# Optimization experiments

Hardware: AMD Instinct MI355X
Metric: run time of the kernel (lower is better)

Reference implementation:

```python
import jax, jax.numpy as jnp
import numpy as np

B, S, N, C = 8, 256, 256, 64
NH = 8
H, W = 256, 256
D = N * C // NH  # per-head channel dim = 2048
EPS = 1e-12


def window_reverse(windows, ws, Hh, Ww, Cc):
    # windows: (B, S, N, C) -> (B, H*W, C)
    b = windows.shape[0]
    x = windows.reshape(b, Hh // ws[0], Ww // ws[1], ws[0], ws[1], Cc)
    x = x.transpose(0, 1, 3, 2, 4, 5).reshape(b, Hh, Ww, Cc).reshape(b, Hh * Ww, Cc)
    return x


def window_partition(x, ws):
    # x: (B, H, W, C) -> (B, nWin, winElems, C)
    b, hh, ww, cc = x.shape
    x = x.reshape(b, hh // ws[0], ws[0], ww // ws[1], ws[1], cc)
    return x.transpose(0, 1, 3, 2, 4, 5).reshape(b, (hh // ws[0]) * (ww // ws[1]), ws[0] * ws[1], cc)


def setup_inputs() -> dict:
    key = jax.random.key(0)
    ks = jax.random.split(key, 6)
    x = jax.random.normal(ks[0], (B, S, N, C), dtype=jnp.float32)
    qkv_w = jax.random.normal(ks[1], (4 * C, C), dtype=jnp.float32) * 0.02
    qkv_b = jnp.zeros((4 * C,), dtype=jnp.float32)
    proj_w = jax.random.normal(ks[2], (C, C), dtype=jnp.float32) * 0.02
    proj_b = jnp.zeros((C,), dtype=jnp.float32)
    temperature1 = jnp.ones((NH, 1, 1), dtype=jnp.float32)
    temperature2 = jnp.ones((NH, 1, 1), dtype=jnp.float32)
    return {"x": x, "qkv_w": qkv_w, "qkv_b": qkv_b, "proj_w": proj_w,
            "proj_b": proj_b, "temperature1": temperature1, "temperature2": temperature2}


def reference(x, qkv_w, qkv_b, proj_w, proj_b, temperature1, temperature2):
    b, s, n, c = x.shape
    xf = x.reshape(b, s * n, c)
    # fused 4-way qkv projection (q, k, v_H, v_V)
    qkvv = (xf @ qkv_w.T + qkv_b).reshape(b, s, 4, NH, D).transpose(2, 0, 3, 1, 4)
    q, k, v_H, v_V = qkvv[0], qkvv[1], qkvv[2], qkvv[3]  # each (B, NH, S, D)

    # reorient v_V from H-windows (columns) to V-windows (rows)
    v_V = v_V.transpose(0, 2, 1, 3).reshape(b, s, n, c)       # (B,S,N,C)
    v_V = v_V.transpose(0, 2, 1, 3)                           # (B,N,S,C)
    v_V = window_reverse(v_V, (H, 1), H, W, c).reshape(b, H, W, c)
    v_V = window_partition(v_V, (1, W))                       # (B,H,W,C)
    v_V = v_V.transpose(0, 2, 1, 3)                           # (B,W,H,C) == (B,S,N,C)
    v_V = v_V.reshape(b, s, NH, D).transpose(0, 2, 1, 3)      # (B,NH,S,D)

    # cosine attention over S with per-head temperature
    qn = q / jnp.maximum(jnp.linalg.norm(q, axis=-1, keepdims=True), EPS)
    kn = k / jnp.maximum(jnp.linalg.norm(k, axis=-1, keepdims=True), EPS)
    sim = jnp.einsum('bhsd,bhtd->bhst', qn, kn)  # (B,NH,S,S)
    attn_H = jax.nn.softmax(sim * temperature1, axis=-1)
    attn_V = jax.nn.softmax(sim * temperature2, axis=-1)

    x_H = jnp.einsum('bhst,bhtd->bhsd', attn_H, v_H).transpose(0, 2, 1, 3).reshape(b, s * n, c)
    x_V = jnp.einsum('bhst,bhtd->bhsd', attn_V, v_V).transpose(0, 2, 1, 3).reshape(b, s * n, c)

    out = (x_H + x_V) @ proj_w.T + proj_b
    return out.reshape(b, s, n, c)
```

## Files before the change

### kernel.cpp

```cpp
#include <hip/hip_runtime.h>


using half_t = _Float16;
using half8 = __attribute__((ext_vector_type(8))) _Float16;
using f32x4 = __attribute__((ext_vector_type(4))) float;

#define NTOK 524288

#define GLDS(g, l) __builtin_amdgcn_global_load_lds( \
    (const __attribute__((address_space(1))) void*)(g), \
    (__attribute__((address_space(3))) void*)(l), 16, 0, 0)

#define WS_Q      0
#define WS_K      67108864
#define WS_VH     134217728
#define WS_VV     201326592
#define WS_XHV    268435456
#define WS_NQ     335544320
#define WS_NK     335609856
#define WS_WH     335675392
#define WS_WP     335708160

__global__ void kW0(const float* __restrict__ qkv_w, const float* __restrict__ proj_w,
                    half_t* __restrict__ Wh, half_t* __restrict__ Wp) {
    int tid = threadIdx.x;
    for (int i = tid; i < 256 * 64; i += 256) Wh[i] = (half_t)qkv_w[i];
    for (int i = tid; i < 64 * 64; i += 256) Wp[i] = (half_t)proj_w[i];
}

__device__ inline void y_tile_mfma(const float* __restrict__ xb,
                                   const half_t* __restrict__ Wh,
                                   int tbase, int hi, int lo,
                                   f32x4 (&acc)[4][4], int wave, int lane) {
    const int l15 = lane & 15, quad = lane >> 4;
#pragma unroll
    for (int kc = 0; kc < 2; ++kc) {
        const int c = kc * 32 + quad * 8;
        half8 afr[4];
#pragma unroll
        for (int mt = 0; mt < 4; ++mt) {
            int m = mt * 16 + l15;
            int token = tbase + (m >> 3) * hi + (m & 7) * lo;
            const float* p = xb + (size_t)token * 64 + c;
            f32x4 f0 = *(const f32x4*)p;
            f32x4 f1 = *(const f32x4*)(p + 4);
            half8 a;
            a[0] = (half_t)f0[0]; a[1] = (half_t)f0[1]; a[2] = (half_t)f0[2]; a[3] = (half_t)f0[3];
            a[4] = (half_t)f1[0]; a[5] = (half_t)f1[1]; a[6] = (half_t)f1[2]; a[7] = (half_t)f1[3];
            afr[mt] = a;
        }
#pragma unroll
        for (int i = 0; i < 4; ++i) {
            int j = (wave * 4 + i) * 16 + l15;
            half8 bfr = *(const half8*)(Wh + j * 64 + c);
#pragma unroll
            for (int mt = 0; mt < 4; ++mt)
                acc[mt][i] = __builtin_amdgcn_mfma_f32_16x16x32_f16(afr[mt], bfr, acc[mt][i], 0, 0, 0);
        }
    }
}

__device__ inline void y_dump_rowmajor(f32x4 (&acc)[4][4], const float* __restrict__ qkv_b,
                                       half_t* ylds, int wave, int lane) {
    const int l15 = lane & 15, quad = lane >> 4;
#pragma unroll
    for (int i = 0; i < 4; ++i) {
        int j = (wave * 4 + i) * 16 + l15;
        float bj = qkv_b[j];
#pragma unroll
        for (int mt = 0; mt < 4; ++mt)
#pragma unroll
            for (int r = 0; r < 4; ++r)
                ylds[(mt * 16 + quad * 4 + r) * 264 + j] = (half_t)(acc[mt][i][r] + bj);
    }
}

__device__ inline void y_dump_transposed(f32x4 (&acc)[4][4], const float* __restrict__ qkv_b,
                                         half_t* yldsT, int wave, int lane) {
    const int l15 = lane & 15, quad = lane >> 4;
#pragma unroll
    for (int i = 0; i < 4; ++i) {
        int j = (wave * 4 + i) * 16 + l15;
        float bj = qkv_b[j];
#pragma unroll
        for (int mt = 0; mt < 4; ++mt)
#pragma unroll
            for (int r = 0; r < 4; ++r)
                yldsT[j * 72 + mt * 16 + quad * 4 + r] = (half_t)(acc[mt][i][r] + bj);
    }
}

__global__ __launch_bounds__(256) void kA1(const float* __restrict__ x,
                                           const half_t* __restrict__ Wh,
                                           const float* __restrict__ qkv_b,
                                           half_t* __restrict__ Q, half_t* __restrict__ K,
                                           float* __restrict__ normQ, float* __restrict__ normK) {
    __shared__ half_t ylds[64 * 264];
    __shared__ float scr[256];
    int idx = blockIdx.x;
    int sb = idx & 31; idx >>= 5;
    int h = idx & 7; idx >>= 3;
    int g = idx & 1; int b = idx >> 1;
    int s0 = sb * 8;
    int n0 = g * 64 + h * 8;
    int tid = threadIdx.x, wave = tid >> 6, lane = tid & 63;
    const float* xb = x + (size_t)b * 65536 * 64;
    f32x4 acc[4][4];
#pragma unroll
    for (int a = 0; a < 4; ++a)
#pragma unroll
        for (int c = 0; c < 4; ++c) acc[a][c] = {0.f, 0.f, 0.f, 0.f};
    y_tile_mfma(xb, Wh, s0 * 256 + n0, 256, 1, acc, wave, lane);
    y_dump_rowmajor(acc, qkv_b, ylds, wave, lane);
    __syncthreads();
    half_t* dst = (g == 0 ? Q : K) + ((size_t)(b * 8 + h) * 256 + s0) * 2048;
    int ns = tid >> 5, jc = (tid & 31) * 8;
#pragma unroll
    for (int si = 0; si < 8; ++si) {
        half8 v = *(const half8*)&ylds[(si * 8 + ns) * 264 + jc];
        *(half8*)(dst + (size_t)si * 2048 + ns * 256 + jc) = v;
    }
    float sum = 0.f;
#pragma unroll
    for (int nn = 0; nn < 8; ++nn) {
        half8 v = *(const half8*)&ylds[((tid >> 5) * 8 + nn) * 264 + (tid & 31) * 8];
#pragma unroll
        for (int e = 0; e < 8; ++e) { float f = (float)v[e]; sum += f * f; }
    }
    scr[tid] = sum;
    __syncthreads();
    if (tid < 8) {
        float s = 0.f;
        for (int k2 = 0; k2 < 32; ++k2) s += scr[tid * 32 + k2];
        float* nd = (g == 0 ? normQ : normK);
        nd[(b * 8 + h) * 256 + s0 + tid] = s;
    }
}

__global__ __launch_bounds__(256) void kA2H(const float* __restrict__ x,
                                            const half_t* __restrict__ Wh,
                                            const float* __restrict__ qkv_b,
                                            half_t* __restrict__ VH) {
    __shared__ half_t yldsT[256 * 72];
    int idx = blockIdx.x;
    int sb = idx & 3; idx >>= 2;
    int nn = idx & 63; int b = idx >> 6;
    int h = nn >> 3, ns = nn & 7;
    int n = 128 + nn;
    int s0 = sb * 64;
    int tid = threadIdx.x, wave = tid >> 6, lane = tid & 63;
    const float* xb = x + (size_t)b * 65536 * 64;
    f32x4 acc[4][4];
#pragma unroll
    for (int a = 0; a < 4; ++a)
#pragma unroll
        for (int c = 0; c < 4; ++c) acc[a][c] = {0.f, 0.f, 0.f, 0.f};
    y_tile_mfma(xb, Wh, s0 * 256 + n, 2048, 256, acc, wave, lane);
    y_dump_transposed(acc, qkv_b, yldsT, wave, lane);
    __syncthreads();
    int jl = lane >> 3, tc = lane & 7;
    half_t* base = VH + ((size_t)(b * 8 + h) * 2048 + ns * 256) * 256 + s0 + tc * 8;
#pragma unroll
    for (int u = 0; u < 8; ++u) {
        int j = wave * 64 + u * 8 + jl;
        half8 v = *(const half8*)&yldsT[j * 72 + tc * 8];
        *(half8*)(base + (size_t)j * 256) = v;
    }
}

__global__ __launch_bounds__(256) void kA2V(const float* __restrict__ x,
                                            const half_t* __restrict__ Wh,
                                            const float* __restrict__ qkv_b,
                                            half_t* __restrict__ VV) {
    __shared__ half_t yldsT[256 * 72];
    int idx = blockIdx.x;
    int st = idx & 255; int b = idx >> 8;
    int h = st >> 5;
    int tid = threadIdx.x, wave = tid >> 6, lane = tid & 63;
    const float* xb = x + (size_t)b * 65536 * 64;
    f32x4 acc[4][4];
#pragma unroll
    for (int a = 0; a < 4; ++a)
#pragma unroll
        for (int c = 0; c < 4; ++c) acc[a][c] = {0.f, 0.f, 0.f, 0.f};
    y_tile_mfma(xb, Wh, st * 256 + 192, 8, 1, acc, wave, lane);
    y_dump_transposed(acc, qkv_b, yldsT, wave, lane);
    __syncthreads();
    int dl = lane >> 3, tc = lane & 7;
    int mbase = wave * 16 + (tc >> 2) * 8 + (tc & 3) * 2;
    half_t* base = VV + ((size_t)(b * 8 + h) * 2048 + (st & 31) * 64) * 256 + wave * 64 + tc * 8;
#pragma unroll
    for (int u = 0; u < 8; ++u) {
        int dm = u * 8 + dl;
        half8 v;
#pragma unroll
        for (int e = 0; e < 8; ++e)
            v[e] = yldsT[((e & 3) * 64 + dm) * 72 + mbase + (e >> 2)];
        *(half8*)(base + (size_t)dm * 256) = v;
    }
}

__global__ __launch_bounds__(1024, 4) void kB(const half_t* __restrict__ Q, const half_t* __restrict__ K,
                                              const half_t* __restrict__ VH, const half_t* __restrict__ VV,
                                              const float* __restrict__ normQ, const float* __restrict__ normK,
                                              const float* __restrict__ temp1, const float* __restrict__ temp2,
                                              half_t* __restrict__ xhv) {
    extern __shared__ char smem[];
    char* Ks0 = smem;
    char* Ks1 = smem + 32768;
    char* Qs0 = smem + 65536;
    char* Qs1 = smem + 73728;
    half_t* PH = (half_t*)(smem + 81920);
    half_t* PV = (half_t*)(smem + 115712);
    float* redA = (float*)(smem + 149504);
    float* redB = (float*)(smem + 153600);
    float* mH  = (float*)(smem + 157696);
    float* mV  = (float*)(smem + 157952);
    float* rHs = (float*)(smem + 158208);
    float* rVs = (float*)(smem + 158464);
    float* rq  = (float*)(smem + 158720);
    float* rk  = (float*)(smem + 158976);

    int idx = blockIdx.x;
    int bh = idx & 63;
    int sqb = idx >> 6;
    int h = bh & 7, b = bh >> 3;
    int sq0 = sqb * 64;
    int tid = threadIdx.x, wave = tid >> 6, lane = tid & 63;
    int l15 = lane & 15, quad = lane >> 4;
    float t1 = temp1[h], t2 = temp2[h];
    const half_t* Qb = Q + (size_t)bh * 256 * 2048;
    const half_t* Kb = K + (size_t)bh * 256 * 2048;
    const half_t* VHb = VH + (size_t)bh * 2048 * 256;
    const half_t* VVb = VV + (size_t)bh * 2048 * 256;

    if (tid < 64) rq[tid] = 1.f / fmaxf(sqrtf(normQ[bh * 256 + sq0 + tid]), 1e-12f);
    if (tid < 256) rk[tid] = 1.f / fmaxf(sqrtf(normK[bh * 256 + tid]), 1e-12f);

    {
        const int l7 = lane & 7, l8 = lane >> 3;
        const int swzh = (l7 ^ (l8 & 7)) * 8;
        const half_t* gK0 = Kb + (size_t)(wave * 8 + l8) * 2048 + swzh;
        const half_t* gK1 = Kb + (size_t)(128 + wave * 8 + l8) * 2048 + swzh;
        const half_t* gQ  = Qb + (size_t)(sq0 + (wave & 7) * 8 + l8) * 2048 + swzh;

        auto STAGE = [&](int kk, char* KsB, char* QsB) {
            const int off = kk * 64;
            GLDS(gK0 + off, KsB + wave * 1024);
            GLDS(gK1 + off, KsB + 16384 + wave * 1024);
            if (wave < 8) GLDS(gQ + off, QsB + wave * 1024);
        };

        f32x4 acc1[4];
#pragma unroll
        for (int a = 0; a < 4; ++a) acc1[a] = {0.f, 0.f, 0.f, 0.f};
        const int tcol = wave * 16 + l15;
        const int ts7 = tcol & 7;

        auto COMPUTE = [&](const char* KsB_, const char* QsB_) {
            const half_t* KsB = (const half_t*)KsB_;
            const half_t* QsB = (const half_t*)QsB_;
#pragma unroll
            for (int sub = 0; sub < 2; ++sub) {
                int c16 = sub * 4 + quad;
                half8 bfr = *(const half8*)(KsB + tcol * 64 + (c16 ^ ts7) * 8);
#pragma unroll
                for (int mt = 0; mt < 4; ++mt) {
                    int m = mt * 16 + l15;
                    half8 afr = *(const half8*)(QsB + m * 64 + (c16 ^ (m & 7)) * 8);
                    acc1[mt] = __builtin_amdgcn_mfma_f32_16x16x32_f16(afr, bfr, acc1[mt], 0, 0, 0);
                }
            }
        };

        STAGE(0, Ks0, Qs0);
        __syncthreads();
        for (int kk = 0; kk < 32; kk += 2) {
            if (kk + 1 < 32) STAGE(kk + 1, Ks1, Qs1);
            COMPUTE(Ks0, Qs0);
            __syncthreads();
            if (kk + 2 < 32) STAGE(kk + 2, Ks0, Qs0);
            COMPUTE(Ks1, Qs1);
            __syncthreads();
        }
        float rkt = rk[tcol];
#pragma unroll
        for (int mt = 0; mt < 4; ++mt)
#pragma unroll
            for (int r = 0; r < 4; ++r) {
                int row = mt * 16 + quad * 4 + r;
                PH[row * 264 + tcol] = (half_t)(acc1[mt][r] * rq[row] * rkt);
            }
    }
    __syncthreads();

    int r_ = tid & 63, cc = tid >> 6;
    half_t* phrow = &PH[r_ * 264 + cc * 16];
    half_t* pvrow = &PV[r_ * 264 + cc * 16];
    float mx = -3.4e38f, mn = 3.4e38f;
#pragma unroll
    for (int i2 = 0; i2 < 16; ++i2) { float v = (float)phrow[i2]; mx = fmaxf(mx, v); mn = fminf(mn, v); }
    redA[tid] = mx; redB[tid] = mn;
    __syncthreads();
    if (tid < 64) {
        float amx = -3.4e38f, amn = 3.4e38f;
#pragma unroll
        for (int q2 = 0; q2 < 16; ++q2) {
            amx = fmaxf(amx, redA[q2 * 64 + tid]);
            amn = fminf(amn, redB[q2 * 64 + tid]);
        }
        mH[tid] = (t1 >= 0.f) ? t1 * amx : t1 * amn;
        mV[tid] = (t2 >= 0.f) ? t2 * amx : t2 * amn;
    }
    __syncthreads();
    float mh = mH[r_], mv = mV[r_];
    float sh = 0.f, sv = 0.f;
#pragma unroll
    for (int i2 = 0; i2 < 16; ++i2) {
        float v = (float)phrow[i2];
        sh += __expf(v * t1 - mh);
        sv += __expf(v * t2 - mv);
    }
    redA[tid] = sh; redB[tid] = sv;
    __syncthreads();
    if (tid < 64) {
        float ash = 0.f, asv = 0.f;
#pragma unroll
        for (int q2 = 0; q2 < 16; ++q2) { ash += redA[q2 * 64 + tid]; asv += redB[q2 * 64 + tid]; }
        rHs[tid] = 1.f / ash;
        rVs[tid] = 1.f / asv;
    }
    __syncthreads();
    float rh = rHs[r_], rv = rVs[r_];
#pragma unroll
    for (int i2 = 0; i2 < 16; ++i2) {
        float v = (float)phrow[i2];
        phrow[i2] = (half_t)(__expf(v * t1 - mh) * rh);
        pvrow[i2] = (half_t)(__expf(v * t2 - mv) * rv);
    }
    __syncthreads();

#pragma unroll
    for (int i2 = 0; i2 < 2; ++i2) {
        int d0 = wave * 64 + i2 * 1024;
        f32x4 acc2[4][4];
#pragma unroll
        for (int a = 0; a < 4; ++a)
#pragma unroll
            for (int c = 0; c < 4; ++c) acc2[a][c] = {0.f, 0.f, 0.f, 0.f};
        for (int kc = 0; kc < 8; ++kc) {
            int tk = kc * 32 + quad * 8;
            half8 afr[4];
#pragma unroll
            for (int mt = 0; mt < 4; ++mt)
                afr[mt] = *(const half8*)&PH[(mt * 16 + l15) * 264 + tk];
#pragma unroll
            for (int nt = 0; nt < 4; ++nt) {
                half8 bfr = *(const half8*)(VHb + (size_t)(d0 + nt * 16 + l15) * 256 + tk);
#pragma unroll
                for (int mt = 0; mt < 4; ++mt)
                    acc2[mt][nt] = __builtin_amdgcn_mfma_f32_16x16x32_f16(afr[mt], bfr, acc2[mt][nt], 0, 0, 0);
            }
#pragma unroll
            for (int mt = 0; mt < 4; ++mt)
                afr[mt] = *(const half8*)&PV[(mt * 16 + l15) * 264 + tk];
#pragma unroll
            for (int nt = 0; nt < 4; ++nt) {
                half8 bfr = *(const half8*)(VVb + (size_t)(d0 + nt * 16 + l15) * 256 + tk);
#pragma unroll
                for (int mt = 0; mt < 4; ++mt)
                    acc2[mt][nt] = __builtin_amdgcn_mfma_f32_16x16x32_f16(afr[mt], bfr, acc2[mt][nt], 0, 0, 0);
            }
        }
        int db = wave + i2 * 16;
#pragma unroll
        for (int mt = 0; mt < 4; ++mt)
#pragma unroll
            for (int nt = 0; nt < 4; ++nt) {
                int c = nt * 16 + l15;
#pragma unroll
                for (int r = 0; r < 4; ++r) {
                    int srow = mt * 16 + quad * 4 + r;
                    size_t tk_idx = (size_t)b * 65536 + (size_t)(sq0 + srow) * 256 + h * 32 + db;
                    xhv[tk_idx * 64 + c] = (half_t)acc2[mt][nt][r];
                }
            }
    }
}

__global__ __launch_bounds__(256) void kC(const half_t* __restrict__ xhv, const half_t* __restrict__ Wp,
                                          const float* __restrict__ proj_b, float* __restrict__ out) {
    __shared__ float ot[64 * 68];
    int tid = threadIdx.x, wave = tid >> 6, lane = tid & 63;
    int l15 = lane & 15, quad = lane >> 4;
    size_t T0 = (size_t)blockIdx.x * 64;
    f32x4 acc[4];
#pragma unroll
    for (int a = 0; a < 4; ++a) acc[a] = {0.f, 0.f, 0.f, 0.f};
#pragma unroll
    for (int kc = 0; kc < 2; ++kc) {
        int c = kc * 32 + quad * 8;
        half8 bfr = *(const half8*)(Wp + (wave * 16 + l15) * 64 + c);
#pragma unroll
        for (int mt = 0; mt < 4; ++mt) {
            half8 afr = *(const half8*)(xhv + (T0 + mt * 16 + l15) * 64 + c);
            acc[mt] = __builtin_amdgcn_mfma_f32_16x16x32_f16(afr, bfr, acc[mt], 0, 0, 0);
        }
    }
    float bj = proj_b[wave * 16 + l15];
#pragma unroll
    for (int mt = 0; mt < 4; ++mt)
#pragma unroll
        for (int r = 0; r < 4; ++r)
            ot[(mt * 16 + quad * 4 + r) * 68 + wave * 16 + l15] = acc[mt][r] + bj;
    __syncthreads();
    int row = tid >> 2;
#pragma unroll
    for (int u = 0; u < 4; ++u) {
        int col = (tid & 3) * 4 + u * 16;
        f32x4 v = *(const f32x4*)&ot[row * 68 + col];
        *(f32x4*)(out + (T0 + row) * 64 + col) = v;
    }
}

extern "C" void kernel_launch(void* const* d_in, const int* in_sizes, int n_in,
                              void* d_out, int out_size, void* d_ws, size_t ws_size,
                              hipStream_t stream) {
    const float* x      = (const float*)d_in[0];
    const float* qkv_w  = (const float*)d_in[1];
    const float* qkv_b  = (const float*)d_in[2];
    const float* proj_w = (const float*)d_in[3];
    const float* proj_b = (const float*)d_in[4];
    const float* temp1  = (const float*)d_in[5];
    const float* temp2  = (const float*)d_in[6];
    char* ws = (char*)d_ws;
    half_t* Q   = (half_t*)(ws + WS_Q);
    half_t* K   = (half_t*)(ws + WS_K);
    half_t* VH  = (half_t*)(ws + WS_VH);
    half_t* VV  = (half_t*)(ws + WS_VV);
    half_t* xhv = (half_t*)(ws + WS_XHV);
    float* normQ = (float*)(ws + WS_NQ);
    float* normK = (float*)(ws + WS_NK);
    half_t* Wh  = (half_t*)(ws + WS_WH);
    half_t* Wp  = (half_t*)(ws + WS_WP);
    float* out = (float*)d_out;

    hipFuncSetAttribute((const void*)kB, hipFuncAttributeMaxDynamicSharedMemorySize, 160000);

    kW0<<<1, 256, 0, stream>>>(qkv_w, proj_w, Wh, Wp);
    kA1<<<4096, 256, 0, stream>>>(x, Wh, qkv_b, Q, K, normQ, normK);
    kA2H<<<2048, 256, 0, stream>>>(x, Wh, qkv_b, VH);
    kA2V<<<2048, 256, 0, stream>>>(x, Wh, qkv_b, VV);
    kB<<<256, 1024, 160000, stream>>>(Q, K, VH, VV, normQ, normK, temp1, temp2, xhv);
    kC<<<8192, 256, 0, stream>>>(xhv, Wp, proj_b, out);
}
```

Before: 605.9 us.

## Fuse output projection into attention kernel and use shuffle-based softmax

Removes the separate projection kernel by applying proj_w per 16-row tile inside the attention kernel, staging the fp16 tile in reused LDS and writing fp32 output directly. This eliminates the intermediate xhv buffer's global write and read and one launch. The softmax reductions now use 16-lane shuffles instead of LDS reductions with multiple barriers. The output stores become narrower per lane, and the attention kernel uses more registers.

```diff
diff --git a/kernel.cpp b/kernel.cpp
--- a/kernel.cpp
+++ b/kernel.cpp
@@ -15,7 +15,6 @@
 #define WS_K      67108864
 #define WS_VH     134217728
 #define WS_VV     201326592
-#define WS_XHV    268435456
 #define WS_NQ     335544320
 #define WS_NK     335609856
 #define WS_WH     335675392
@@ -204,22 +203,18 @@
                                               const half_t* __restrict__ VH, const half_t* __restrict__ VV,
                                               const float* __restrict__ normQ, const float* __restrict__ normK,
                                               const float* __restrict__ temp1, const float* __restrict__ temp2,
-                                              half_t* __restrict__ xhv) {
+                                              const half_t* __restrict__ Wp, const float* __restrict__ proj_b,
+                                              float* __restrict__ out) {
     extern __shared__ char smem[];
     char* Ks0 = smem;
     char* Ks1 = smem + 32768;
     char* Qs0 = smem + 65536;
     char* Qs1 = smem + 73728;
+    half_t* scratch = (half_t*)smem;
     half_t* PH = (half_t*)(smem + 81920);
     half_t* PV = (half_t*)(smem + 115712);
-    float* redA = (float*)(smem + 149504);
-    float* redB = (float*)(smem + 153600);
-    float* mH  = (float*)(smem + 157696);
-    float* mV  = (float*)(smem + 157952);
-    float* rHs = (float*)(smem + 158208);
-    float* rVs = (float*)(smem + 158464);
-    float* rq  = (float*)(smem + 158720);
-    float* rk  = (float*)(smem + 158976);
+    float* rq  = (float*)(smem + 149504);
+    float* rk  = (float*)(smem + 149760);
 
     int idx = blockIdx.x;
     int bh = idx & 63;
@@ -294,51 +289,54 @@
     }
     __syncthreads();
 
-    int r_ = tid & 63, cc = tid >> 6;
-    half_t* phrow = &PH[r_ * 264 + cc * 16];
-    half_t* pvrow = &PV[r_ * 264 + cc * 16];
-    float mx = -3.4e38f, mn = 3.4e38f;
-#pragma unroll
-    for (int i2 = 0; i2 < 16; ++i2) { float v = (float)phrow[i2]; mx = fmaxf(mx, v); mn = fminf(mn, v); }
-    redA[tid] = mx; redB[tid] = mn;
-    __syncthreads();
-    if (tid < 64) {
-        float amx = -3.4e38f, amn = 3.4e38f;
-#pragma unroll
-        for (int q2 = 0; q2 < 16; ++q2) {
-            amx = fmaxf(amx, redA[q2 * 64 + tid]);
-            amn = fminf(amn, redB[q2 * 64 + tid]);
-        }
-        mH[tid] = (t1 >= 0.f) ? t1 * amx : t1 * amn;
-        mV[tid] = (t2 >= 0.f) ? t2 * amx : t2 * amn;
-    }
-    __syncthreads();
-    float mh = mH[r_], mv = mV[r_];
-    float sh = 0.f, sv = 0.f;
-#pragma unroll
-    for (int i2 = 0; i2 < 16; ++i2) {
-        float v = (float)phrow[i2];
-        sh += __expf(v * t1 - mh);
-        sv += __expf(v * t2 - mv);
-    }
-    redA[tid] = sh; redB[tid] = sv;
-    __syncthreads();
-    if (tid < 64) {
-        float ash = 0.f, asv = 0.f;
-#pragma unroll
-        for (int q2 = 0; q2 < 16; ++q2) { ash += redA[q2 * 64 + tid]; asv += redB[q2 * 64 + tid]; }
-        rHs[tid] = 1.f / ash;
-        rVs[tid] = 1.f / asv;
-    }
-    __syncthreads();
-    float rh = rHs[r_], rv = rVs[r_];
-#pragma unroll
-    for (int i2 = 0; i2 < 16; ++i2) {
-        float v = (float)phrow[i2];
-        phrow[i2] = (half_t)(__expf(v * t1 - mh) * rh);
-        pvrow[i2] = (half_t)(__expf(v * t2 - mv) * rv);
-    }
-    __syncthreads();
+    {
+        int r_ = tid >> 4, cc = tid & 15;
+        half_t* phrow = &PH[r_ * 264 + cc * 16];
+        half_t* pvrow = &PV[r_ * 264 + cc * 16];
+        half8 v0 = *(const half8*)phrow;
+        half8 v1 = *(const half8*)(phrow + 8);
+        float fv[16];
+#pragma unroll
+        for (int e = 0; e < 8; ++e) { fv[e] = (float)v0[e]; fv[8 + e] = (float)v1[e]; }
+        float mx = fv[0], mn = fv[0];
+#pragma unroll
+        for (int e = 1; e < 16; ++e) { mx = fmaxf(mx, fv[e]); mn = fminf(mn, fv[e]); }
+#pragma unroll
+        for (int m = 1; m < 16; m <<= 1) {
+            mx = fmaxf(mx, __shfl_xor(mx, m, 16));
+            mn = fminf(mn, __shfl_xor(mn, m, 16));
+        }
+        float mh = (t1 >= 0.f) ? t1 * mx : t1 * mn;
+        float mv = (t2 >= 0.f) ? t2 * mx : t2 * mn;
+        float sh = 0.f, sv = 0.f;
+#pragma unroll
+        for (int e = 0; e < 16; ++e) {
+            sh += __expf(fv[e] * t1 - mh);
+            sv += __expf(fv[e] * t2 - mv);
+        }
+#pragma unroll
+        for (int m = 1; m < 16; m <<= 1) {
+            sh += __shfl_xor(sh, m, 16);
+            sv += __shfl_xor(sv, m, 16);
+        }
+        float rh = 1.f / sh, rv = 1.f / sv;
+        half8 o0, o1, p0, p1;
+#pragma unroll
+        for (int e = 0; e < 8; ++e) {
+            o0[e] = (half_t)(__expf(fv[e] * t1 - mh) * rh);
+            o1[e] = (half_t)(__expf(fv[8 + e] * t1 - mh) * rh);
+            p0[e] = (half_t)(__expf(fv[e] * t2 - mv) * rv);
+            p1[e] = (half_t)(__expf(fv[8 + e] * t2 - mv) * rv);
+        }
+        *(half8*)phrow = o0; *(half8*)(phrow + 8) = o1;
+        *(half8*)pvrow = p0; *(half8*)(pvrow + 8) = p1;
+    }
+    __syncthreads();
+
+    half_t* myscr = scratch + wave * 1152;
+    float bj[4];
+#pragma unroll
+    for (int jt = 0; jt < 4; ++jt) bj[jt] = proj_b[jt * 16 + l15];
 
 #pragma unroll
     for (int i2 = 0; i2 < 2; ++i2) {
@@ -374,52 +372,33 @@
         }
         int db = wave + i2 * 16;
 #pragma unroll
-        for (int mt = 0; mt < 4; ++mt)
-#pragma unroll
-            for (int nt = 0; nt < 4; ++nt) {
-                int c = nt * 16 + l15;
+        for (int mt = 0; mt < 4; ++mt) {
+#pragma unroll
+            for (int nt = 0; nt < 4; ++nt)
+#pragma unroll
+                for (int r = 0; r < 4; ++r)
+                    myscr[(quad * 4 + r) * 72 + nt * 16 + l15] = (half_t)acc2[mt][nt][r];
+            f32x4 accp[4];
+#pragma unroll
+            for (int jt = 0; jt < 4; ++jt) accp[jt] = {0.f, 0.f, 0.f, 0.f};
+#pragma unroll
+            for (int kc2 = 0; kc2 < 2; ++kc2) {
+                half8 afr = *(const half8*)&myscr[l15 * 72 + kc2 * 32 + quad * 8];
+#pragma unroll
+                for (int jt = 0; jt < 4; ++jt) {
+                    half8 bfr = *(const half8*)(Wp + (jt * 16 + l15) * 64 + kc2 * 32 + quad * 8);
+                    accp[jt] = __builtin_amdgcn_mfma_f32_16x16x32_f16(afr, bfr, accp[jt], 0, 0, 0);
+                }
+            }
+#pragma unroll
+            for (int jt = 0; jt < 4; ++jt)
 #pragma unroll
                 for (int r = 0; r < 4; ++r) {
                     int srow = mt * 16 + quad * 4 + r;
-                    size_t tk_idx = (size_t)b * 65536 + (size_t)(sq0 + srow) * 256 + h * 32 + db;
-                    xhv[tk_idx * 64 + c] = (half_t)acc2[mt][nt][r];
+                    size_t token = (size_t)b * 65536 + (size_t)(sq0 + srow) * 256 + h * 32 + db;
+                    out[token * 64 + jt * 16 + l15] = accp[jt][r] + bj[jt];
                 }
-            }
-    }
-}
-
-__global__ __launch_bounds__(256) void kC(const half_t* __restrict__ xhv, const half_t* __restrict__ Wp,
-                                          const float* __restrict__ proj_b, float* __restrict__ out) {
-    __shared__ float ot[64 * 68];
-    int tid = threadIdx.x, wave = tid >> 6, lane = tid & 63;
-    int l15 = lane & 15, quad = lane >> 4;
-    size_t T0 = (size_t)blockIdx.x * 64;
-    f32x4 acc[4];
-#pragma unroll
-    for (int a = 0; a < 4; ++a) acc[a] = {0.f, 0.f, 0.f, 0.f};
-#pragma unroll
-    for (int kc = 0; kc < 2; ++kc) {
-        int c = kc * 32 + quad * 8;
-        half8 bfr = *(const half8*)(Wp + (wave * 16 + l15) * 64 + c);
-#pragma unroll
-        for (int mt = 0; mt < 4; ++mt) {
-            half8 afr = *(const half8*)(xhv + (T0 + mt * 16 + l15) * 64 + c);
-            acc[mt] = __builtin_amdgcn_mfma_f32_16x16x32_f16(afr, bfr, acc[mt], 0, 0, 0);
-        }
-    }
-    float bj = proj_b[wave * 16 + l15];
-#pragma unroll
-    for (int mt = 0; mt < 4; ++mt)
-#pragma unroll
-        for (int r = 0; r < 4; ++r)
-            ot[(mt * 16 + quad * 4 + r) * 68 + wave * 16 + l15] = acc[mt][r] + bj;
-    __syncthreads();
-    int row = tid >> 2;
-#pragma unroll
-    for (int u = 0; u < 4; ++u) {
-        int col = (tid & 3) * 4 + u * 16;
-        f32x4 v = *(const f32x4*)&ot[row * 68 + col];
-        *(f32x4*)(out + (T0 + row) * 64 + col) = v;
+        }
     }
 }
 
@@ -438,19 +417,18 @@
     half_t* K   = (half_t*)(ws + WS_K);
     half_t* VH  = (half_t*)(ws + WS_VH);
     half_t* VV  = (half_t*)(ws + WS_VV);
-    half_t* xhv = (half_t*)(ws + WS_XHV);
     float* normQ = (float*)(ws + WS_NQ);
     float* normK = (float*)(ws + WS_NK);
     half_t* Wh  = (half_t*)(ws + WS_WH);
     half_t* Wp  = (half_t*)(ws + WS_WP);
     float* out = (float*)d_out;
 
-    hipFuncSetAttribute((const void*)kB, hipFuncAttributeMaxDynamicSharedMemorySize, 160000);
+    hipFuncSetAttribute((const void*)kB, hipFuncAttributeMaxDynamicSharedMemorySize, 150784);
 
     kW0<<<1, 256, 0, stream>>>(qkv_w, proj_w, Wh, Wp);
     kA1<<<4096, 256, 0, stream>>>(x, Wh, qkv_b, Q, K, normQ, normK);
     kA2H<<<2048, 256, 0, stream>>>(x, Wh, qkv_b, VH);
     kA2V<<<2048, 256, 0, stream>>>(x, Wh, qkv_b, VV);
-    kB<<<256, 1024, 160000, stream>>>(Q, K, VH, VV, normQ, normK, temp1, temp2, xhv);
-    kC<<<8192, 256, 0, stream>>>(xhv, Wp, proj_b, out);
-}
+    kB<<<256, 1024, 150784, stream>>>(Q, K, VH, VV, normQ, normK, temp1, temp2,
+                                      Wp, proj_b, out);
+}
```

Measured after the change: 618.2 us. 2.0% more time.
